# Kernel tuning notes

Measured on AMD Instinct MI355X. Metric: run time of the kernel, lower is better.

Reference implementation:

```python
import jax, jax.numpy as jnp
import numpy as np

N_NODES = 50000
N_EDGES = 800000
D_IN = 64
D_OUT = 64
N_REL = 8


def setup_inputs() -> dict:
    key = jax.random.key(0)
    ks = jax.random.split(key, 7)
    x = jax.random.normal(ks[0], (N_NODES, D_IN), jnp.float32)
    src = jax.random.randint(ks[1], (N_EDGES,), 0, N_NODES)   # neighbor ids
    dst = jax.random.randint(ks[2], (N_EDGES,), 0, N_NODES)   # center node ids
    rel = jax.random.randint(ks[3], (N_EDGES,), 0, N_REL)
    # xavier_uniform for W_r: [R, 2*d, d]
    lim = float(np.sqrt(6.0 / (2 * D_IN + D_IN)))
    W_r = jax.random.uniform(ks[4], (N_REL, 2 * D_IN, D_IN), jnp.float32, -lim, lim)
    # nn.Linear(2*d, d_out): weight [d_out, 2*d], bias [d_out]
    lim2 = float(1.0 / np.sqrt(2 * D_IN))
    W_lin = jax.random.uniform(ks[5], (D_OUT, 2 * D_IN), jnp.float32, -lim2, lim2)
    b_lin = jax.random.uniform(ks[6], (D_OUT,), jnp.float32, -lim2, lim2)
    return {"x": x, "src": src, "dst": dst, "rel": rel,
            "W_r": W_r, "W_lin": W_lin, "b_lin": b_lin}


def reference(x, src, dst, rel, W_r, W_lin, b_lin):
    n, d = x.shape
    e = src.shape[0]
    # gate logit per edge: (concat(x[dst], x[src]) @ W_r[rel]).sum(-1)
    # == concat(x[dst], x[src]) . W_r[rel].sum(-1)  -- mathematically identical,
    # avoids materializing the [E, 2d, d] matmul the torch loop performs.
    w = W_r.sum(-1)                      # [R, 2d]
    w_dst, w_src = w[:, :d], w[:, d:]    # [R, d] each
    logit = jnp.sum(x[dst] * w_dst[rel], axis=-1) + jnp.sum(x[src] * w_src[rel], axis=-1)  # [E]
    gate = jax.nn.sigmoid(logit)[:, None]        # [E, 1]
    weighted = x[src] * gate                     # [E, d]
    # scatter-mean over destination nodes (nodes with no edges stay zero)
    agg_sum = jax.ops.segment_sum(weighted, dst, num_segments=n)            # [N, d]
    cnt = jax.ops.segment_sum(jnp.ones((e,), x.dtype), dst, num_segments=n)  # [N]
    agg = agg_sum / jnp.maximum(cnt, 1.0)[:, None]
    combined = jnp.concatenate([x, agg], axis=-1)  # [N, 2d]
    out = combined @ W_lin.T + b_lin               # [N, d_out]
    return jax.nn.leaky_relu(out, negative_slope=0.01)
```

## Files before the change

### kernel.cpp

```cpp
#include <hip/hip_runtime.h>
#include <hip/hip_fp16.h>
#include <cmath>

#define N_NODES 50000
#define N_EDGES 800000
#define D 64
#define N_REL 8

#define NODES_PER_BLK 32
#define TN 16
#define MAXDEG 64
#define NSEG 8
#define SEG_DIV 6250

static __device__ __forceinline__ unsigned f2bf(float f) {
    unsigned u = __float_as_uint(f);
    return (u + 0x7FFFu + ((u >> 16) & 1u)) >> 16;
}
#define BFLO(u) __uint_as_float((u) << 16)
#define BFHI(u) __uint_as_float((u) & 0xFFFF0000u)

__global__ void wprep_kernel(const float* __restrict__ W_r, float* __restrict__ w,
                             int* __restrict__ cnt) {
    int t = blockIdx.x * blockDim.x + threadIdx.x;
    if (t < N_REL * 2 * D) {
        const float* p = W_r + (size_t)t * D;
        float s = 0.0f;
#pragma unroll
        for (int k = 0; k < D; ++k) s += p[k];
        w[t] = s;
    }
    for (int i = t; i < N_NODES; i += gridDim.x * blockDim.x)
        cnt[i] = 0;
}

__global__ __launch_bounds__(256) void tables_kernel(
    const float* __restrict__ x, const float* __restrict__ w,
    float* __restrict__ Dn, float* __restrict__ Sr,
    unsigned short* __restrict__ xb)
{
    __shared__ float xs[TN][68];
    __shared__ float ws[16][68];

    int tid = threadIdx.x;
    int n0  = blockIdx.x * TN;

    for (int i = tid; i < 16 * 64; i += 256)
        ws[i >> 6][i & 63] = w[i];
    for (int i = tid; i < TN * 64; i += 256) {
        int n = n0 + (i >> 6);
        xs[i >> 6][i & 63] = (n < N_NODES) ? x[(size_t)n * D + (i & 63)] : 0.f;
    }
    __syncthreads();

    for (int i = tid; i < TN * 64; i += 256) {
        int n = n0 + (i >> 6);
        if (n < N_NODES) xb[(size_t)n0 * D + i] = (unsigned short)f2bf(xs[i >> 6][i & 63]);
    }

    int q = tid & 15, nl = tid >> 4;
    float acc = 0.f;
#pragma unroll
    for (int k = 0; k < 64; k += 4) {
        float4 a = *(const float4*)&xs[nl][k];
        float4 b = *(const float4*)&ws[q][k];
        acc += a.x * b.x + a.y * b.y + a.z * b.z + a.w * b.w;
    }
    int n = n0 + nl;
    if (n < N_NODES) {
        int r = q >> 1;
        if ((q & 1) == 0) Dn[n * 8 + r] = acc;
        else              Sr[n * 8 + r] = acc;
    }
}

__global__ __launch_bounds__(256) void scatter_kernel(
    const int* __restrict__ src, const int* __restrict__ dst,
    const int* __restrict__ rel,
    int* __restrict__ cnt,
    const float* __restrict__ Dn, const float* __restrict__ Sr,
    unsigned int* __restrict__ epack) {
    int seg   = blockIdx.x & (NSEG - 1);
    int chunk = blockIdx.x >> 3;
    int e = chunk * 256 + threadIdx.x;
    if (e >= N_EDGES) return;

    int d = dst[e];
    int s = src[e];
    int r = rel[e];
    asm volatile("" :: "v"(d), "v"(s), "v"(r));

    if ((unsigned)d / SEG_DIV != (unsigned)seg) return;

    int rank = atomicAdd(&cnt[d], 1);

    float logit = Dn[d * 8 + r] + Sr[s * 8 + r];
    float gate = 1.0f / (1.0f + __expf(-logit));
    if (rank < MAXDEG) {
        unsigned pv = ((unsigned)__half_as_ushort(__float2half_rn(gate)) << 16)
                    | (unsigned)s;
        epack[(size_t)d * MAXDEG + rank] = pv;
    }
}

__global__ __launch_bounds__(256) void agglin_kernel(
    const unsigned short* __restrict__ xb,
    const unsigned int* __restrict__ xbu,
    const int*   __restrict__ cnt,
    const unsigned int* __restrict__ epack,
    const float* __restrict__ W_lin,
    const float* __restrict__ b_lin,
    float* __restrict__ out)
{
    __shared__ unsigned int W2[64][66];
    __shared__ unsigned int c2[NODES_PER_BLK][66];
    __shared__ float b_lds[64];

    int tid  = threadIdx.x;
    int n0   = blockIdx.x * NODES_PER_BLK;
    int lane = tid & 63;
    int wv   = tid >> 6;

    for (int i = tid; i < 64 * 64; i += 256) {
        int j = i >> 6, kp = i & 63;
        float2 wvv = *(const float2*)&W_lin[j * 128 + kp * 2];
        W2[j][kp] = f2bf(wvv.x) | (f2bf(wvv.y) << 16);
    }
    if (tid < 64) b_lds[tid] = b_lin[tid];

    for (int i = tid; i < NODES_PER_BLK * 32; i += 256) {
        int nl = i >> 5, kp = i & 31;
        int n  = n0 + nl;
        c2[nl][kp] = (n < N_NODES) ? xbu[(size_t)n * 32 + kp] : 0u;
    }

    int nbase = n0 + wv * 8;

    int      degv[8];
    unsigned ev[8];
#pragma unroll
    for (int i = 0; i < 8; ++i) {
        int n = nbase + i;
        degv[i] = (n < N_NODES) ? cnt[n] : 0;
    }
#pragma unroll
    for (int i = 0; i < 8; ++i) {
        int n = nbase + i;
        ev[i] = (n < N_NODES) ? epack[(size_t)n * MAXDEG + lane] : 0u;
    }

    int sub = lane >> 4;
    int q   = lane & 15;
    int q4  = q * 4;

#pragma unroll
    for (int i = 0; i < 8; ++i) {
        int m = (degv[i] < MAXDEG) ? degv[i] : MAXDEG;
        unsigned e_m = (lane < m) ? ev[i] : 0u;
        float gl = __half2float(__ushort_as_half((unsigned short)(e_m >> 16)));
        int   ol = (int)(e_m & 0xFFFFu) * D;

        float ax = 0.f, ay = 0.f, az = 0.f, aw = 0.f;
        for (int base = 0; base < m; base += 8) {
            int e0 = base + sub;
            int e1 = base + 4 + sub;
            float g0 = __shfl(gl, e0, 64);
            int   o0 = __shfl(ol, e0, 64);
            float g1 = __shfl(gl, e1, 64);
            int   o1 = __shfl(ol, e1, 64);
            uint2 u0 = *(const uint2*)&xb[(size_t)o0 + q4];
            uint2 u1 = *(const uint2*)&xb[(size_t)o1 + q4];
            ax += g0 * BFLO(u0.x) + g1 * BFLO(u1.x);
            ay += g0 * BFHI(u0.x) + g1 * BFHI(u1.x);
            az += g0 * BFLO(u0.y) + g1 * BFLO(u1.y);
            aw += g0 * BFHI(u0.y) + g1 * BFHI(u1.y);
        }

#pragma unroll
        for (int off = 16; off <= 32; off <<= 1) {
            ax += __shfl_xor(ax, off, 64);
            ay += __shfl_xor(ay, off, 64);
            az += __shfl_xor(az, off, 64);
            aw += __shfl_xor(aw, off, 64);
        }

        if (sub == 0) {
            float inv = 1.0f / fmaxf((float)degv[i], 1.0f);
            int nl = wv * 8 + i;
            c2[nl][32 + 2 * q]     = f2bf(ax * inv) | (f2bf(ay * inv) << 16);
            c2[nl][32 + 2 * q + 1] = f2bf(az * inv) | (f2bf(aw * inv) << 16);
        }
    }
    __syncthreads();

    int tx = tid & 15, ty = tid >> 4;
    float acc[2][4];
#pragma unroll
    for (int i = 0; i < 2; ++i)
#pragma unroll
        for (int jj = 0; jj < 4; ++jj) acc[i][jj] = b_lds[tx + 16 * jj];

#pragma unroll 2
    for (int kp = 0; kp < 64; kp += 2) {
        uint2 cu[2], wu[4];
        cu[0] = *(const uint2*)&c2[ty][kp];
        cu[1] = *(const uint2*)&c2[ty + 16][kp];
#pragma unroll
        for (int jj = 0; jj < 4; ++jj)
            wu[jj] = *(const uint2*)&W2[tx + 16 * jj][kp];
#pragma unroll
        for (int i = 0; i < 2; ++i) {
            float cx = BFLO(cu[i].x), cy = BFHI(cu[i].x);
            float cz = BFLO(cu[i].y), cw = BFHI(cu[i].y);
#pragma unroll
            for (int jj = 0; jj < 4; ++jj) {
                acc[i][jj] += cx * BFLO(wu[jj].x) + cy * BFHI(wu[jj].x)
                            + cz * BFLO(wu[jj].y) + cw * BFHI(wu[jj].y);
            }
        }
    }

#pragma unroll
    for (int i = 0; i < 2; ++i) {
        int n = n0 + ty + 16 * i;
        if (n < N_NODES) {
#pragma unroll
            for (int jj = 0; jj < 4; ++jj) {
                float v = acc[i][jj];
                out[(size_t)n * D + tx + 16 * jj] = (v > 0.f) ? v : 0.01f * v;
            }
        }
    }
}

extern "C" void kernel_launch(void* const* d_in, const int* in_sizes, int n_in,
                              void* d_out, int out_size, void* d_ws, size_t ws_size,
                              hipStream_t stream) {
    const float* x     = (const float*)d_in[0];
    const int*   src   = (const int*)  d_in[1];
    const int*   dst   = (const int*)  d_in[2];
    const int*   rel   = (const int*)  d_in[3];
    const float* W_r   = (const float*)d_in[4];
    const float* W_lin = (const float*)d_in[5];
    const float* b_lin = (const float*)d_in[6];
    float* out = (float*)d_out;

    char* p = (char*)d_ws;
    float*  w       = (float*)p;                p += 4096;
    float*  Dn      = (float*)p;                p += (size_t)N_NODES * 8 * 4;
    float*  Sr      = (float*)p;                p += (size_t)N_NODES * 8 * 4;
    int*    cnt     = (int*)p;                  p += 256 * 1024;
    unsigned int* epack = (unsigned int*)p;     p += (size_t)N_NODES * MAXDEG * 4;
    unsigned short* xb = (unsigned short*)p;    p += (size_t)N_NODES * D * 2;

    wprep_kernel<<<512, 256, 0, stream>>>(W_r, w, cnt);
    tables_kernel<<<(N_NODES + TN - 1) / TN, 256, 0, stream>>>(x, w, Dn, Sr, xb);
    scatter_kernel<<<NSEG * ((N_EDGES + 255) / 256), 256, 0, stream>>>(
        src, dst, rel, cnt, Dn, Sr, epack);
    agglin_kernel<<<(N_NODES + NODES_PER_BLK - 1) / NODES_PER_BLK, 256, 0, stream>>>(
        xb, (const unsigned int*)xb, cnt, epack, W_lin, b_lin, out);
}
```

Before: 177.4 us.

## Use MFMA bf16 for final linear and drop segmented scatter passes

Replaces the scalar FMA 32x64x128 GEMM tail of the aggregation kernel with bf16 MFMA 16x16x32 instructions and pads the LDS rows to 68 words so the 16-byte fragment loads stay aligned. It also removes the 8-way destination-segmented scatter launch, which read every edge eight times to get L2 locality on atomics, and uses a single pass over the edges instead. The single pass cuts redundant edge reads and launch work, but it makes the atomics and epack writes fully random across all nodes. The bounds check is dropped because the edge count divides exactly by 256.

```diff
diff --git a/kernel.cpp b/kernel.cpp
--- a/kernel.cpp
+++ b/kernel.cpp
@@ -10,8 +10,10 @@
 #define NODES_PER_BLK 32
 #define TN 16
 #define MAXDEG 64
-#define NSEG 8
-#define SEG_DIV 6250
+
+typedef __attribute__((ext_vector_type(8))) short bf16x8;
+typedef __attribute__((ext_vector_type(4))) float f32x4;
+union FragU { uint4 u; bf16x8 b; };
 
 static __device__ __forceinline__ unsigned f2bf(float f) {
     unsigned u = __float_as_uint(f);
@@ -80,17 +82,11 @@
     int* __restrict__ cnt,
     const float* __restrict__ Dn, const float* __restrict__ Sr,
     unsigned int* __restrict__ epack) {
-    int seg   = blockIdx.x & (NSEG - 1);
-    int chunk = blockIdx.x >> 3;
-    int e = chunk * 256 + threadIdx.x;
-    if (e >= N_EDGES) return;
+    int e = blockIdx.x * 256 + threadIdx.x;
 
     int d = dst[e];
     int s = src[e];
     int r = rel[e];
-    asm volatile("" :: "v"(d), "v"(s), "v"(r));
-
-    if ((unsigned)d / SEG_DIV != (unsigned)seg) return;
 
     int rank = atomicAdd(&cnt[d], 1);
 
@@ -112,8 +108,8 @@
     const float* __restrict__ b_lin,
     float* __restrict__ out)
 {
-    __shared__ unsigned int W2[64][66];
-    __shared__ unsigned int c2[NODES_PER_BLK][66];
+    __shared__ unsigned int W2[64][68];
+    __shared__ unsigned int c2[NODES_PER_BLK][68];
     __shared__ float b_lds[64];
 
     int tid  = threadIdx.x;
@@ -193,42 +189,35 @@
     }
     __syncthreads();
 
-    int tx = tid & 15, ty = tid >> 4;
-    float acc[2][4];
-#pragma unroll
-    for (int i = 0; i < 2; ++i)
-#pragma unroll
-        for (int jj = 0; jj < 4; ++jj) acc[i][jj] = b_lds[tx + 16 * jj];
-
-#pragma unroll 2
-    for (int kp = 0; kp < 64; kp += 2) {
-        uint2 cu[2], wu[4];
-        cu[0] = *(const uint2*)&c2[ty][kp];
-        cu[1] = *(const uint2*)&c2[ty + 16][kp];
-#pragma unroll
-        for (int jj = 0; jj < 4; ++jj)
-            wu[jj] = *(const uint2*)&W2[tx + 16 * jj][kp];
-#pragma unroll
-        for (int i = 0; i < 2; ++i) {
-            float cx = BFLO(cu[i].x), cy = BFHI(cu[i].x);
-            float cz = BFLO(cu[i].y), cw = BFHI(cu[i].y);
-#pragma unroll
-            for (int jj = 0; jj < 4; ++jj) {
-                acc[i][jj] += cx * BFLO(wu[jj].x) + cy * BFHI(wu[jj].x)
-                            + cz * BFLO(wu[jj].y) + cw * BFHI(wu[jj].y);
-            }
-        }
-    }
-
-#pragma unroll
-    for (int i = 0; i < 2; ++i) {
-        int n = n0 + ty + 16 * i;
-        if (n < N_NODES) {
-#pragma unroll
-            for (int jj = 0; jj < 4; ++jj) {
-                float v = acc[i][jj];
-                out[(size_t)n * D + tx + 16 * jj] = (v > 0.f) ? v : 0.01f * v;
-            }
+    int mtile = wv & 1;
+    int nt0   = wv >> 1;
+    int lrow  = lane & 15;
+    int kgrp  = lane >> 4;
+
+    float bias0 = b_lds[nt0 * 16 + lrow];
+    float bias1 = b_lds[(nt0 + 2) * 16 + lrow];
+    f32x4 acc0 = {bias0, bias0, bias0, bias0};
+    f32x4 acc1 = {bias1, bias1, bias1, bias1};
+
+#pragma unroll
+    for (int ks = 0; ks < 4; ++ks) {
+        int cb = ks * 16 + kgrp * 4;
+        FragU a, b0, b1;
+        a.u  = *(const uint4*)&c2[mtile * 16 + lrow][cb];
+        b0.u = *(const uint4*)&W2[nt0 * 16 + lrow][cb];
+        b1.u = *(const uint4*)&W2[(nt0 + 2) * 16 + lrow][cb];
+        acc0 = __builtin_amdgcn_mfma_f32_16x16x32_bf16(a.b, b0.b, acc0, 0, 0, 0);
+        acc1 = __builtin_amdgcn_mfma_f32_16x16x32_bf16(a.b, b1.b, acc1, 0, 0, 0);
+    }
+
+#pragma unroll
+    for (int i = 0; i < 4; ++i) {
+        int node = n0 + mtile * 16 + kgrp * 4 + i;
+        if (node < N_NODES) {
+            float v0 = acc0[i]; v0 = (v0 > 0.f) ? v0 : 0.01f * v0;
+            float v1 = acc1[i]; v1 = (v1 > 0.f) ? v1 : 0.01f * v1;
+            out[(size_t)node * D + nt0 * 16 + lrow]       = v0;
+            out[(size_t)node * D + (nt0 + 2) * 16 + lrow] = v1;
         }
     }
 }
@@ -255,7 +244,7 @@
 
     wprep_kernel<<<512, 256, 0, stream>>>(W_r, w, cnt);
     tables_kernel<<<(N_NODES + TN - 1) / TN, 256, 0, stream>>>(x, w, Dn, Sr, xb);
-    scatter_kernel<<<NSEG * ((N_EDGES + 255) / 256), 256, 0, stream>>>(
+    scatter_kernel<<<N_EDGES / 256, 256, 0, stream>>>(
         src, dst, rel, cnt, Dn, Sr, epack);
     agglin_kernel<<<(N_NODES + NODES_PER_BLK - 1) / NODES_PER_BLK, 256, 0, stream>>>(
         xb, (const unsigned int*)xb, cnt, epack, W_lin, b_lin, out);
```

New measurement: 169.0 us. 4.7% less time.
